# Optimization experiments

Hardware: AMD Instinct MI355X
Metric: run time of the kernel (lower is better)

Reference implementation:

```python
import jax, jax.numpy as jnp
import numpy as np

N_NODES = 10000
N_EDGES = 160000
K = 3  # Chebyshev filter order
DIMS = [(782, 16), (16, 32), (32, 64), (64, 128), (128, 19)]


def _cheb_norm(edge_index, num_nodes):
    # PyG ChebConv norm with normalization='sym', lambda_max=2.0:
    # scaled Laplacian L_hat = 2L/lambda_max - I = -D^{-1/2} A D^{-1/2} (off-diag), diag = 0
    src, dst = edge_index[0], edge_index[1]
    w = jnp.ones(src.shape, dtype=jnp.float32)
    deg = jax.ops.segment_sum(w, src, num_segments=num_nodes)
    dinv = jnp.where(deg > 0, 1.0 / jnp.sqrt(deg), 0.0)  # masked_fill(inf) -> 0
    return -dinv[src] * dinv[dst]


def _spmm(norm, src, dst, x, num_nodes):
    # out[i] = sum_{e: dst[e]==i} norm[e] * x[src[e]]
    return jax.ops.segment_sum(norm[:, None] * x[src], dst, num_segments=num_nodes)


def _cheb_conv(x, src, dst, norm, W, b):
    # W: [K, Fin, Fout]; Chebyshev recursion T0=x, T1=L_hat x, Tk=2 L_hat T_{k-1} - T_{k-2}
    n = x.shape[0]
    Tx0 = x
    out = Tx0 @ W[0]
    Tx1 = _spmm(norm, src, dst, Tx0, n)
    out = out + Tx1 @ W[1]
    for k in range(2, W.shape[0]):
        Tx2 = 2.0 * _spmm(norm, src, dst, Tx1, n) - Tx0
        out = out + Tx2 @ W[k]
        Tx0, Tx1 = Tx1, Tx2
    return out + b


def setup_inputs() -> dict:
    key = jax.random.key(0)
    ks = jax.random.split(key, 2 + len(DIMS))
    x = jax.random.normal(ks[0], (N_NODES, 782), dtype=jnp.float32)
    edge_index = jax.random.randint(ks[1], (2, N_EDGES), 0, N_NODES)
    inp = {"x": x, "edge_index": edge_index}
    for i, (fi, fo) in enumerate(DIMS):
        inp[f"W{i+1}"] = jax.random.normal(ks[2 + i], (K, fi, fo), dtype=jnp.float32) / np.float32(np.sqrt(fi * K))
        inp[f"b{i+1}"] = jnp.zeros((fo,), dtype=jnp.float32)
    return inp


def reference(x, edge_index, W1, b1, W2, b2, W3, b3, W4, b4, W5, b5):
    src, dst = edge_index[0], edge_index[1]
    norm = _cheb_norm(edge_index, x.shape[0])
    h = jax.nn.relu(_cheb_conv(x, src, dst, norm, W1, b1))
    h = jax.nn.relu(_cheb_conv(h, src, dst, norm, W2, b2))
    h = jax.nn.relu(_cheb_conv(h, src, dst, norm, W3, b3))
    h = jax.nn.relu(_cheb_conv(h, src, dst, norm, W4, b4))
    h = _cheb_conv(h, src, dst, norm, W5, b5)
    return jax.nn.softmax(h, axis=-1)
```

## Files before the change

### kernel.cpp

```cpp
#include <hip/hip_runtime.h>
#include <math.h>

#define NN 10000
#define NE 160000
#define CAP 128
#define NT 256
#define WC1_TOTAL (782 * 48)
#define WC5_TOTAL (128 * 60)
#define L1_SPLITS 12
#define L1_KCHUNK 66
#define L1_TN 24
#define L1_RT 4
#define L1_TILES 240
#define CNT_BLKS 625

struct MegaParams {
  const float* x;
  const int* src;
  const int* dst;
  const float* W1; const float* b1;
  const float* W2; const float* b2;
  const float* W3; const float* b3;
  const float* W4; const float* b4;
  const float* W5; const float* b5;
  int* deg; int* cnt; int* bsrc;
  float* dinv; float* wc1; float* wc5;
  float* ABC1; float* E1; float* B2; float* B3; float* B4;
  float* H4; float* ABC5; float* E5; float* P;
  float* out;
};

__device__ __forceinline__ void wcat_one(const float* __restrict__ W,
                                         float* __restrict__ Wc,
                                         int i, int Fin, int F, int Fp) {
  int w3 = 3 * Fp;
  int row = i / w3;
  int c = i - row * w3;
  int sec = c / Fp;
  int f = c - sec * Fp;
  float v = 0.0f;
  if (f < F) {
    if (sec == 0)      v = W[row * F + f] - W[2 * Fin * F + row * F + f];
    else if (sec == 1) v = W[Fin * F + row * F + f];
    else               v = W[2 * Fin * F + row * F + f];
  }
  Wc[i] = v;
}

struct Row8 { float4 lo, hi; };

template <bool AL16>
__device__ __forceinline__ Row8 ld_row8(const float* __restrict__ X, int ldx,
                                        int gr, int M, int kc, int kend) {
  Row8 r;
  r.lo = make_float4(0.f, 0.f, 0.f, 0.f);
  r.hi = make_float4(0.f, 0.f, 0.f, 0.f);
  if (gr < M && kc < kend) {
    const float* xp = X + (size_t)gr * ldx + kc;
    if (kc + 8 <= kend) {
      if (AL16) {
        r.lo = ((const float4*)xp)[0];
        r.hi = ((const float4*)xp)[1];
      } else {
        float2 a = *(const float2*)xp;
        float2 b = *(const float2*)(xp + 2);
        float2 c = *(const float2*)(xp + 4);
        float2 d = *(const float2*)(xp + 6);
        r.lo = make_float4(a.x, a.y, b.x, b.y);
        r.hi = make_float4(c.x, c.y, d.x, d.y);
      }
    } else {
      int rem = kend - kc;
      r.lo.x = xp[0];
      if (rem > 1) r.lo.y = xp[1];
      if (rem > 2) r.lo.z = xp[2];
      if (rem > 3) r.lo.w = xp[3];
      if (rem > 4) r.hi.x = xp[4];
      if (rem > 5) r.hi.y = xp[5];
      if (rem > 6) r.hi.z = xp[6];
    }
  }
  return r;
}

__device__ __forceinline__ float comp8(const Row8& r, int k) {
  switch (k) {
    case 0: return r.lo.x; case 1: return r.lo.y;
    case 2: return r.lo.z; case 3: return r.lo.w;
    case 4: return r.hi.x; case 5: return r.hi.y;
    case 6: return r.hi.z; default: return r.hi.w;
  }
}

template <int TN, int RT, bool AL16, bool DIRECT>
__device__ void gemm_stage(const float* __restrict__ X, int ldx,
                           const float* __restrict__ W, int ldw,
                           float* __restrict__ Y, int ldy,
                           const float* __restrict__ bias, int relu,
                           int M, int Kd, int Nd, int kchunk, int nk,
                           int tile0, int tstride, float* Ws) {
  constexpr int RTILE = NT * RT;
  int ntR = (M + RTILE - 1) / RTILE;
  int ntC = Nd / TN;
  int ntRC = ntR * ntC;
  int ntiles = ntRC * nk;
  constexpr int W4 = TN / 4;
  for (int tile = tile0; tile < ntiles; tile += tstride) {
    int tz = tile / ntRC;
    int rm = tile - tz * ntRC;
    int tc = rm / ntR;
    int tr = rm - tc * ntR;
    int row0 = tr * RTILE;
    int col0 = tc * TN;
    int k0 = tz * kchunk;
    int kend = k0 + kchunk;
    if (kend > Kd) kend = Kd;
    int k8 = ((kend - k0) + 7) & ~7;
    __syncthreads();
    for (int idx = threadIdx.x; idx < k8 * W4; idx += NT) {
      int wk = idx / W4;
      int wc = (idx - wk * W4) * 4;
      float4 wv = make_float4(0.f, 0.f, 0.f, 0.f);
      if (k0 + wk < kend)
        wv = *(const float4*)(W + (size_t)(k0 + wk) * ldw + col0 + wc);
      *(float4*)(Ws + wk * TN + wc) = wv;
    }
    __syncthreads();
    float acc[RT][TN];
#pragma unroll
    for (int i = 0; i < RT; i++)
#pragma unroll
      for (int c = 0; c < TN; c++) acc[i][c] = 0.f;
    int nch = k8 >> 3;
    Row8 cur[RT], nxt[RT];
#pragma unroll
    for (int i = 0; i < RT; i++)
      cur[i] = ld_row8<AL16>(X, ldx, row0 + threadIdx.x + i * NT, M, k0, kend);
    for (int ci = 0; ci < nch; ci++) {
#pragma unroll
      for (int i = 0; i < RT; i++) nxt[i] = cur[i];
      if (ci + 1 < nch) {
#pragma unroll
        for (int i = 0; i < RT; i++)
          nxt[i] = ld_row8<AL16>(X, ldx, row0 + threadIdx.x + i * NT, M,
                                 k0 + (ci + 1) * 8, kend);
      }
      int kb = ci << 3;
#pragma unroll
      for (int k = 0; k < 8; k++) {
        float x0[RT];
#pragma unroll
        for (int i = 0; i < RT; i++) x0[i] = comp8(cur[i], k);
        const float* wr = Ws + (kb + k) * TN;
#pragma unroll
        for (int c = 0; c < TN; c += 4) {
          float4 wv = *(const float4*)(wr + c);
#pragma unroll
          for (int i = 0; i < RT; i++) {
            acc[i][c + 0] += x0[i] * wv.x; acc[i][c + 1] += x0[i] * wv.y;
            acc[i][c + 2] += x0[i] * wv.z; acc[i][c + 3] += x0[i] * wv.w;
          }
        }
      }
#pragma unroll
      for (int i = 0; i < RT; i++) cur[i] = nxt[i];
    }
#pragma unroll
    for (int i = 0; i < RT; i++) {
      int r = row0 + threadIdx.x + i * NT;
      if (r < M) {
        if (DIRECT) {
          float* yr = Y + (size_t)r * ldy + col0;
#pragma unroll
          for (int c = 0; c < TN; c += 4) {
            float4 v;
            v.x = acc[i][c + 0] + (bias ? bias[col0 + c + 0] : 0.f);
            v.y = acc[i][c + 1] + (bias ? bias[col0 + c + 1] : 0.f);
            v.z = acc[i][c + 2] + (bias ? bias[col0 + c + 2] : 0.f);
            v.w = acc[i][c + 3] + (bias ? bias[col0 + c + 3] : 0.f);
            if (relu) {
              v.x = fmaxf(v.x, 0.f); v.y = fmaxf(v.y, 0.f);
              v.z = fmaxf(v.z, 0.f); v.w = fmaxf(v.w, 0.f);
            }
            *(float4*)(yr + c) = v;
          }
        } else {
          float* pr = Y + ((size_t)tz * M + r) * Nd + col0;
#pragma unroll
          for (int c = 0; c < TN; c += 4)
            *(float4*)(pr + c) =
                make_float4(acc[i][c], acc[i][c + 1], acc[i][c + 2], acc[i][c + 3]);
        }
      }
    }
  }
}

__device__ void spmm_stage(const int* __restrict__ cnt,
                           const int* __restrict__ bsrc,
                           const float* __restrict__ dinv,
                           const float* __restrict__ X, int ldx,
                           float* __restrict__ Y, int ldy,
                           const float* __restrict__ add, int lda,
                           const float* __restrict__ bias,
                           float alpha, float beta,
                           int C_log2, int Fstore, int relu, int do_softmax) {
  int wv = threadIdx.x >> 6;
  int lane = threadIdx.x & 63;
  int C = 1 << C_log2;
  int chunk = lane & (C - 1);
  int eslot = lane >> C_log2;
  int Epar = 64 >> C_log2;
  for (int node = blockIdx.x * 4 + wv; node < NN; node += gridDim.x * 4) {
    int cn = cnt[node]; if (cn > CAP) cn = CAP;
    float dn = dinv[node];
    int j0 = node << 7;
    int j1 = j0 + cn;
    float sx = 0.f, sy = 0.f, sz = 0.f, sw = 0.f;
    for (int j = j0 + eslot; j < j1; j += Epar) {
      int sn = bsrc[j];
      float w = dinv[sn];
      float4 xv = *(const float4*)(X + (size_t)sn * ldx + (chunk << 2));
      sx += w * xv.x; sy += w * xv.y; sz += w * xv.z; sw += w * xv.w;
    }
    for (int st = C; st < 64; st <<= 1) {
      sx += __shfl_xor(sx, st);
      sy += __shfl_xor(sy, st);
      sz += __shfl_xor(sz, st);
      sw += __shfl_xor(sw, st);
    }
    if (eslot == 0) {
      float am = -alpha * dn;
      int f0 = chunk << 2;
      float4 u = make_float4(am * sx, am * sy, am * sz, am * sw);
      if (add) {
        float4 av = *(const float4*)(add + (size_t)node * lda + f0);
        u.x += beta * av.x; u.y += beta * av.y; u.z += beta * av.z; u.w += beta * av.w;
      }
      if (bias) {
        if (f0 + 0 < Fstore) u.x += bias[f0 + 0];
        if (f0 + 1 < Fstore) u.y += bias[f0 + 1];
        if (f0 + 2 < Fstore) u.z += bias[f0 + 2];
        if (f0 + 3 < Fstore) u.w += bias[f0 + 3];
      }
      if (!do_softmax) {
        if (relu) {
          u.x = fmaxf(u.x, 0.f); u.y = fmaxf(u.y, 0.f);
          u.z = fmaxf(u.z, 0.f); u.w = fmaxf(u.w, 0.f);
        }
        if (f0 + 4 <= Fstore) {
          *(float4*)(Y + (size_t)node * ldy + f0) = u;
        } else {
          float vv[4] = {u.x, u.y, u.z, u.w};
#pragma unroll
          for (int c = 0; c < 4; c++)
            if (f0 + c < Fstore) Y[(size_t)node * ldy + f0 + c] = vv[c];
        }
      } else {
        float v[4] = {u.x, u.y, u.z, u.w};
        float mx = -INFINITY;
#pragma unroll
        for (int c = 0; c < 4; c++)
          if (f0 + c < Fstore) mx = fmaxf(mx, v[c]);
        mx = fmaxf(mx, __shfl_xor(mx, 1));
        mx = fmaxf(mx, __shfl_xor(mx, 2));
        mx = fmaxf(mx, __shfl_xor(mx, 4));
        float e[4];
        float s = 0.f;
#pragma unroll
        for (int c = 0; c < 4; c++) {
          e[c] = (f0 + c < Fstore) ? __expf(v[c] - mx) : 0.f;
          s += e[c];
        }
        s += __shfl_xor(s, 1);
        s += __shfl_xor(s, 2);
        s += __shfl_xor(s, 4);
        float inv = 1.f / s;
#pragma unroll
        for (int c = 0; c < 4; c++) {
          int f = f0 + c;
          if (f < Fstore) Y[(size_t)node * ldy + f] = e[c] * inv;
        }
      }
    }
  }
}


__global__ __launch_bounds__(NT) void k_zero_wcat(MegaParams p) {
  int tid = blockIdx.x * NT + threadIdx.x;
  int TT = gridDim.x * NT;
  for (int i = tid; i < 2 * NN; i += TT) p.deg[i] = 0;
  for (int i = tid; i < WC1_TOTAL; i += TT) wcat_one(p.W1, p.wc1, i, 782, 16, 16);
  for (int i = tid; i < WC5_TOTAL; i += TT) wcat_one(p.W5, p.wc5, i, 128, 19, 20);
}

__global__ __launch_bounds__(NT) void k_count_gemm1(MegaParams p) {
  __shared__ float Ws[72 * L1_TN];
  if (blockIdx.x < CNT_BLKS) {
    int e = blockIdx.x * NT + threadIdx.x;
    int s = p.src[e], d = p.dst[e];
    atomicAdd(&p.deg[s], 1);
    int slot = atomicAdd(&p.cnt[d], 1);
    if (slot < CAP) p.bsrc[(d << 7) + slot] = s;
  } else {
    gemm_stage<L1_TN, L1_RT, false, false>(p.x, 782, p.wc1, 48, p.P, 0, nullptr, 0,
                                           NN, 782, 48, L1_KCHUNK, L1_SPLITS,
                                           blockIdx.x - CNT_BLKS, 1 << 30, Ws);
  }
}

__global__ __launch_bounds__(NT) void k_reduce_dinv(MegaParams p) {
  int tid = blockIdx.x * NT + threadIdx.x;
  int TT = gridDim.x * NT;
  for (int i = tid; i < NN; i += TT) {
    int d = p.deg[i];
    p.dinv[i] = d > 0 ? 1.0f / sqrtf((float)d) : 0.0f;
  }
  for (int i = tid; i < NN * 48; i += TT) {
    float s = 0.f;
#pragma unroll
    for (int z = 0; z < L1_SPLITS; z++) s += p.P[(size_t)z * (NN * 48) + i];
    p.ABC1[i] = s;
  }
}

__global__ __launch_bounds__(NT) void k_spmm(
    const int* cnt, const int* bsrc, const float* dinv,
    const float* X, int ldx, float* Y, int ldy,
    const float* add, int lda, const float* bias,
    float alpha, float beta, int C_log2, int Fstore, int relu, int do_softmax) {
  spmm_stage(cnt, bsrc, dinv, X, ldx, Y, ldy, add, lda, bias,
             alpha, beta, C_log2, Fstore, relu, do_softmax);
}

__global__ __launch_bounds__(NT, 2) void k_gemm32(
    const float* X, int ldx, const float* W, int ldw, float* Y, int ldy,
    const float* bias, int relu, int Kd, int Nd) {
  __shared__ float Ws[96 * 32];
  gemm_stage<32, 1, true, true>(X, ldx, W, ldw, Y, ldy, bias, relu,
                                NN, Kd, Nd, Kd, 1, blockIdx.x, gridDim.x, Ws);
}
__global__ __launch_bounds__(NT, 2) void k_gemm16(
    const float* X, int ldx, const float* W, int ldw, float* Y, int ldy,
    const float* bias, int relu, int Kd, int Nd) {
  __shared__ float Ws[192 * 16];
  gemm_stage<16, 2, true, true>(X, ldx, W, ldw, Y, ldy, bias, relu,
                                NN, Kd, Nd, Kd, 1, blockIdx.x, gridDim.x, Ws);
}
__global__ __launch_bounds__(NT, 2) void k_gemm20(
    const float* X, int ldx, const float* W, int ldw, float* Y, int ldy,
    const float* bias, int relu, int Kd, int Nd) {
  __shared__ float Ws[128 * 20];
  gemm_stage<20, 1, true, true>(X, ldx, W, ldw, Y, ldy, bias, relu,
                                NN, Kd, Nd, Kd, 1, blockIdx.x, gridDim.x, Ws);
}


extern "C" void kernel_launch(void* const* d_in, const int* in_sizes, int n_in,
                              void* d_out, int out_size, void* d_ws, size_t ws_size,
                              hipStream_t stream) {
  (void)in_sizes; (void)n_in; (void)out_size; (void)ws_size;
  char* p = (char*)d_ws;
  auto alloc = [&](size_t bytes) {
    char* r = p;
    p += (bytes + 255) & ~(size_t)255;
    return r;
  };
  int*   i_deg  = (int*)alloc(sizeof(int) * NN * 2);
  int*   i_bsrc = (int*)alloc(sizeof(int) * NN * CAP);
  float* f_dinv = (float*)alloc(sizeof(float) * NN);
  float* wc1    = (float*)alloc(sizeof(float) * WC1_TOTAL);
  float* wc5    = (float*)alloc(sizeof(float) * WC5_TOTAL);
  float* R1     = (float*)alloc(sizeof(float) * NN * 96);
  float* R2     = (float*)alloc(sizeof(float) * NN * 192);
  float* R3     = (float*)alloc(sizeof(float) * NN * 128);
  float* P      = (float*)alloc(sizeof(float) * NN * 48 * L1_SPLITS);

  MegaParams mp;
  mp.x   = (const float*)d_in[0];
  const int* ei = (const int*)d_in[1];
  mp.src = ei;
  mp.dst = ei + NE;
  mp.W1 = (const float*)d_in[2];  mp.b1 = (const float*)d_in[3];
  mp.W2 = (const float*)d_in[4];  mp.b2 = (const float*)d_in[5];
  mp.W3 = (const float*)d_in[6];  mp.b3 = (const float*)d_in[7];
  mp.W4 = (const float*)d_in[8];  mp.b4 = (const float*)d_in[9];
  mp.W5 = (const float*)d_in[10]; mp.b5 = (const float*)d_in[11];
  mp.deg = i_deg; mp.cnt = i_deg + NN; mp.bsrc = i_bsrc;
  mp.dinv = f_dinv; mp.wc1 = wc1; mp.wc5 = wc5;
  mp.ABC1 = R1; mp.B3 = R1; mp.ABC5 = R1;
  mp.E1 = R2;   mp.B4 = R2; mp.E5 = R2;
  mp.B2 = R3;   mp.H4 = R3;
  mp.P = P;
  mp.out = (float*)d_out;

  k_zero_wcat<<<160, NT, 0, stream>>>(mp);
  k_count_gemm1<<<CNT_BLKS + L1_TILES, NT, 0, stream>>>(mp);
  k_reduce_dinv<<<(NN * 48 + NT - 1) / NT, NT, 0, stream>>>(mp);
  k_spmm<<<2500, NT, 0, stream>>>(mp.cnt, mp.bsrc, mp.dinv, mp.ABC1 + 32, 48,
                                  mp.E1, 16, mp.ABC1 + 16, 48, nullptr,
                                  2.f, 1.f, 2, 16, 0, 0);
  k_spmm<<<2500, NT, 0, stream>>>(mp.cnt, mp.bsrc, mp.dinv, mp.E1, 16,
                                  mp.B2, 48, mp.ABC1, 48, mp.b1,
                                  1.f, 1.f, 2, 16, 1, 0);
  k_spmm<<<2500, NT, 0, stream>>>(mp.cnt, mp.bsrc, mp.dinv, mp.B2, 48,
                                  mp.B2 + 16, 48, nullptr, 0, nullptr,
                                  1.f, 0.f, 2, 16, 0, 0);
  k_spmm<<<2500, NT, 0, stream>>>(mp.cnt, mp.bsrc, mp.dinv, mp.B2 + 16, 48,
                                  mp.B2 + 32, 48, mp.B2, 48, nullptr,
                                  2.f, -1.f, 2, 16, 0, 0);
  k_gemm32<<<40, NT, 0, stream>>>(mp.B2, 48, mp.W2, 32, mp.B3, 96, mp.b2, 1, 48, 32);
  k_spmm<<<2500, NT, 0, stream>>>(mp.cnt, mp.bsrc, mp.dinv, mp.B3, 96,
                                  mp.B3 + 32, 96, nullptr, 0, nullptr,
                                  1.f, 0.f, 3, 32, 0, 0);
  k_spmm<<<2500, NT, 0, stream>>>(mp.cnt, mp.bsrc, mp.dinv, mp.B3 + 32, 96,
                                  mp.B3 + 64, 96, mp.B3, 96, nullptr,
                                  2.f, -1.f, 3, 32, 0, 0);
  k_gemm32<<<80, NT, 0, stream>>>(mp.B3, 96, mp.W3, 64, mp.B4, 192, mp.b3, 1, 96, 64);
  k_spmm<<<2500, NT, 0, stream>>>(mp.cnt, mp.bsrc, mp.dinv, mp.B4, 192,
                                  mp.B4 + 64, 192, nullptr, 0, nullptr,
                                  1.f, 0.f, 4, 64, 0, 0);
  k_spmm<<<2500, NT, 0, stream>>>(mp.cnt, mp.bsrc, mp.dinv, mp.B4 + 64, 192,
                                  mp.B4 + 128, 192, mp.B4, 192, nullptr,
                                  2.f, -1.f, 4, 64, 0, 0);
  k_gemm16<<<160, NT, 0, stream>>>(mp.B4, 192, mp.W4, 128, mp.H4, 128, mp.b4, 1,
                                   192, 128);
  k_gemm20<<<120, NT, 0, stream>>>(mp.H4, 128, mp.wc5, 60, mp.ABC5, 60, nullptr, 0,
                                   128, 60);
  k_spmm<<<2500, NT, 0, stream>>>(mp.cnt, mp.bsrc, mp.dinv, mp.ABC5 + 40, 60,
                                  mp.E5, 32, mp.ABC5 + 20, 60, nullptr,
                                  2.f, 1.f, 3, 20, 0, 0);
  k_spmm<<<2500, NT, 0, stream>>>(mp.cnt, mp.bsrc, mp.dinv, mp.E5, 32,
                                  mp.out, 19, mp.ABC5, 60, mp.b5,
                                  1.f, 1.f, 3, 19, 0, 1);
}
```

Before: 288.7 us.

## Replace layer-1 GEMM with register-resident readlane kernel and retile gemm16

The first-layer x·Wcat GEMM (782→48) now uses a dedicated routine. Each wave owns 12 output columns and 4 rows per lane, broadcasts weights across lanes with readlane instead of staging them in shared memory, and double-buffers the X and W loads in registers. The K split goes from 12 chunks of 66 to 13 chunks of 64, which gives more tiles. Separately, gemm16 drops to one row per thread and launches twice as many blocks. The readlane broadcasts add scalar-path instructions, and the register pressure of the 48 accumulators may limit occupancy.

```diff
diff --git a/kernel.cpp b/kernel.cpp
--- a/kernel.cpp
+++ b/kernel.cpp
@@ -7,11 +7,9 @@
 #define NT 256
 #define WC1_TOTAL (782 * 48)
 #define WC5_TOTAL (128 * 60)
-#define L1_SPLITS 12
-#define L1_KCHUNK 66
-#define L1_TN 24
-#define L1_RT 4
-#define L1_TILES 240
+#define L1_SPLITS 13
+#define L1_KCHUNK 64
+#define L1_TILES (40 * L1_SPLITS)
 #define CNT_BLKS 625
 
 struct MegaParams {
@@ -89,6 +87,93 @@
     case 2: return r.lo.z; case 3: return r.lo.w;
     case 4: return r.hi.x; case 5: return r.hi.y;
     case 6: return r.hi.z; default: return r.hi.w;
+  }
+}
+
+__device__ __forceinline__ float rlane(float v, int i) {
+  return __int_as_float(__builtin_amdgcn_readlane(__float_as_int(v), i));
+}
+
+__device__ __forceinline__ float2 ldw8(const float* __restrict__ Wf, int kb,
+                                       int col0, int lc, int lk) {
+  float2 w = make_float2(0.f, 0.f);
+  if (lc < 12) {
+    int k1 = kb + lk, k2 = kb + 4 + lk;
+    if (k1 < 782) w.x = Wf[k1 * 48 + col0 + lc];
+    if (k2 < 782) w.y = Wf[k2 * 48 + col0 + lc];
+  }
+  return w;
+}
+
+__device__ void gemm1_rl(const float* __restrict__ X,
+                         const float* __restrict__ Wf,
+                         float* __restrict__ P,
+                         int tile0, int tstride) {
+  const int ntR = 40;
+  int wid  = threadIdx.x >> 6;
+  int lane = threadIdx.x & 63;
+  int col0 = wid * 12;
+  int lc = lane & 15;
+  int lk = lane >> 4;
+  for (int tile = tile0; tile < ntR * L1_SPLITS; tile += tstride) {
+    int tz = tile / ntR;
+    int tr = tile - tz * ntR;
+    int row0 = tr * 256;
+    int k0 = tz * L1_KCHUNK;
+    int kend = k0 + L1_KCHUNK;
+    if (kend > 782) kend = 782;
+    int nch = ((kend - k0) + 7) >> 3;
+    float acc[4][12];
+#pragma unroll
+    for (int i = 0; i < 4; i++)
+#pragma unroll
+      for (int c = 0; c < 12; c++) acc[i][c] = 0.f;
+    Row8 cur[4], nxt[4];
+    float2 wcur, wnxt;
+#pragma unroll
+    for (int i = 0; i < 4; i++)
+      cur[i] = ld_row8<false>(X, 782, row0 + lane + 64 * i, NN, k0, kend);
+    wcur = ldw8(Wf, k0, col0, lc, lk);
+    for (int ci = 0; ci < nch; ci++) {
+      if (ci + 1 < nch) {
+        int kc2 = k0 + (ci + 1) * 8;
+#pragma unroll
+        for (int i = 0; i < 4; i++)
+          nxt[i] = ld_row8<false>(X, 782, row0 + lane + 64 * i, NN, kc2, kend);
+        wnxt = ldw8(Wf, kc2, col0, lc, lk);
+      }
+#pragma unroll
+      for (int kin = 0; kin < 8; kin++) {
+        float x0 = comp8(cur[0], kin);
+        float x1 = comp8(cur[1], kin);
+        float x2 = comp8(cur[2], kin);
+        float x3 = comp8(cur[3], kin);
+        float wsrc = (kin < 4) ? wcur.x : wcur.y;
+#pragma unroll
+        for (int c = 0; c < 12; c++) {
+          float w = rlane(wsrc, (kin & 3) * 16 + c);
+          acc[0][c] += x0 * w;
+          acc[1][c] += x1 * w;
+          acc[2][c] += x2 * w;
+          acc[3][c] += x3 * w;
+        }
+      }
+      if (ci + 1 < nch) {
+#pragma unroll
+        for (int i = 0; i < 4; i++) cur[i] = nxt[i];
+        wcur = wnxt;
+      }
+    }
+#pragma unroll
+    for (int i = 0; i < 4; i++) {
+      int r = row0 + lane + 64 * i;
+      if (r < NN) {
+        float* pr = P + ((size_t)tz * NN + r) * 48 + col0;
+        *(float4*)(pr + 0) = make_float4(acc[i][0], acc[i][1], acc[i][2], acc[i][3]);
+        *(float4*)(pr + 4) = make_float4(acc[i][4], acc[i][5], acc[i][6], acc[i][7]);
+        *(float4*)(pr + 8) = make_float4(acc[i][8], acc[i][9], acc[i][10], acc[i][11]);
+      }
+    }
   }
 }
 
@@ -296,7 +381,6 @@
 }
 
 __global__ __launch_bounds__(NT) void k_count_gemm1(MegaParams p) {
-  __shared__ float Ws[72 * L1_TN];
   if (blockIdx.x < CNT_BLKS) {
     int e = blockIdx.x * NT + threadIdx.x;
     int s = p.src[e], d = p.dst[e];
@@ -304,9 +388,7 @@
     int slot = atomicAdd(&p.cnt[d], 1);
     if (slot < CAP) p.bsrc[(d << 7) + slot] = s;
   } else {
-    gemm_stage<L1_TN, L1_RT, false, false>(p.x, 782, p.wc1, 48, p.P, 0, nullptr, 0,
-                                           NN, 782, 48, L1_KCHUNK, L1_SPLITS,
-                                           blockIdx.x - CNT_BLKS, 1 << 30, Ws);
+    gemm1_rl(p.x, p.wc1, p.P, blockIdx.x - CNT_BLKS, 1 << 30);
   }
 }
 
@@ -345,7 +427,7 @@
     const float* X, int ldx, const float* W, int ldw, float* Y, int ldy,
     const float* bias, int relu, int Kd, int Nd) {
   __shared__ float Ws[192 * 16];
-  gemm_stage<16, 2, true, true>(X, ldx, W, ldw, Y, ldy, bias, relu,
+  gemm_stage<16, 1, true, true>(X, ldx, W, ldw, Y, ldy, bias, relu,
                                 NN, Kd, Nd, Kd, 1, blockIdx.x, gridDim.x, Ws);
 }
 __global__ __launch_bounds__(NT, 2) void k_gemm20(
@@ -424,7 +506,7 @@
   k_spmm<<<2500, NT, 0, stream>>>(mp.cnt, mp.bsrc, mp.dinv, mp.B4 + 64, 192,
                                   mp.B4 + 128, 192, mp.B4, 192, nullptr,
                                   2.f, -1.f, 4, 64, 0, 0);
-  k_gemm16<<<160, NT, 0, stream>>>(mp.B4, 192, mp.W4, 128, mp.H4, 128, mp.b4, 1,
+  k_gemm16<<<320, NT, 0, stream>>>(mp.B4, 192, mp.W4, 128, mp.H4, 128, mp.b4, 1,
                                    192, 128);
   k_gemm20<<<120, NT, 0, stream>>>(mp.H4, 128, mp.wc5, 60, mp.ABC5, 60, nullptr, 0,
                                    128, 60);
```

New measurement: 275.2 us. 1.05x faster.

## Fuse final Chebyshev SpMM with dense GEMM for layers 2 and 3

Applied to the files above, without the earlier changes.

Adds a fused kernel that computes the T2 SpMM for a node in one wavefront and immediately multiplies the full [T0,T1,T2] row by the weight matrix using readlane broadcasts, applying bias and ReLU. This replaces a separate SpMM and GEMM launch per layer, removing a launch and an intermediate round trip through global memory. It also retunes the layer-1 split-K GEMM to full-width 48-column tiles with twice the blocks, and halves the row tile of the layer-4 GEMM while doubling its grid. The fused kernel keeps each weight column in registers and runs a serial per-node FMA chain, so occupancy and per-node latency may suffer.

```diff
diff --git a/kernel.cpp b/kernel.cpp
--- a/kernel.cpp
+++ b/kernel.cpp
@@ -9,9 +9,6 @@
 #define WC5_TOTAL (128 * 60)
 #define L1_SPLITS 12
 #define L1_KCHUNK 66
-#define L1_TN 24
-#define L1_RT 4
-#define L1_TILES 240
 #define CNT_BLKS 625
 
 struct MegaParams {
@@ -90,6 +87,10 @@
     case 4: return r.hi.x; case 5: return r.hi.y;
     case 6: return r.hi.z; default: return r.hi.w;
   }
+}
+
+__device__ __forceinline__ float rlane(float v, int i) {
+  return __int_as_float(__builtin_amdgcn_readlane(__float_as_int(v), i));
 }
 
 template <int TN, int RT, bool AL16, bool DIRECT>
@@ -286,6 +287,66 @@
   }
 }
 
+template <int F, int C_log2, int LD, int KK, int FOUT, int LDO>
+__global__ __launch_bounds__(NT) void k_fused_t2gemm(
+    const int* __restrict__ cnt, const int* __restrict__ bsrc,
+    const float* __restrict__ dinv, const float* __restrict__ B,
+    const float* __restrict__ W, const float* __restrict__ bias,
+    float* __restrict__ Y) {
+  int wv = threadIdx.x >> 6;
+  int lane = threadIdx.x & 63;
+  constexpr int C = 1 << C_log2;
+  int chunk = lane & (C - 1);
+  int eslot = lane >> C_log2;
+  constexpr int Epar = 64 >> C_log2;
+  int col = lane % FOUT;
+  float wr[KK];
+#pragma unroll
+  for (int k = 0; k < KK; k++) wr[k] = W[k * FOUT + col];
+  float bb = bias[col];
+  for (int node = blockIdx.x * 4 + wv; node < NN; node += gridDim.x * 4) {
+    int cn = cnt[node]; if (cn > CAP) cn = CAP;
+    float dn = dinv[node];
+    int j0 = node << 7, j1 = j0 + cn;
+    float sx = 0.f, sy = 0.f, sz = 0.f, sw = 0.f;
+    for (int j = j0 + eslot; j < j1; j += Epar) {
+      int sn = bsrc[j];
+      float w = dinv[sn];
+      float4 xv = *(const float4*)(B + (size_t)sn * LD + F + (chunk << 2));
+      sx += w * xv.x; sy += w * xv.y; sz += w * xv.z; sw += w * xv.w;
+    }
+#pragma unroll
+    for (int st = C; st < 64; st <<= 1) {
+      sx += __shfl_xor(sx, st);
+      sy += __shfl_xor(sy, st);
+      sz += __shfl_xor(sz, st);
+      sw += __shfl_xor(sw, st);
+    }
+    int ridx = (lane < 2 * F) ? lane : (lane - 2 * F);
+    float rv0 = B[(size_t)node * LD + ridx];
+    int f = (KK == 48) ? (lane - 2 * F) : lane;
+    int cc = (f >> 2) & (C - 1);
+    float a0 = __shfl(sx, cc), a1 = __shfl(sy, cc);
+    float a2 = __shfl(sz, cc), a3 = __shfl(sw, cc);
+    int comp = f & 3;
+    float Ssel = (comp == 0) ? a0 : (comp == 1) ? a1 : (comp == 2) ? a2 : a3;
+    float t2v = fmaf(-2.f * dn, Ssel, -rv0);
+    float acc = bb;
+    if (KK == 48) {
+      float rv = (lane < 2 * F) ? rv0 : t2v;
+#pragma unroll
+      for (int k = 0; k < 48; k++) acc = fmaf(rlane(rv, k), wr[k], acc);
+    } else {
+#pragma unroll
+      for (int k = 0; k < 64; k++) acc = fmaf(rlane(rv0, k), wr[k], acc);
+#pragma unroll
+      for (int k = 64; k < 96; k++) acc = fmaf(rlane(t2v, k - 64), wr[k], acc);
+    }
+    acc = fmaxf(acc, 0.f);
+    if (lane < FOUT) Y[(size_t)node * LDO + col] = acc;
+  }
+}
+
 
 __global__ __launch_bounds__(NT) void k_zero_wcat(MegaParams p) {
   int tid = blockIdx.x * NT + threadIdx.x;
@@ -296,7 +357,7 @@
 }
 
 __global__ __launch_bounds__(NT) void k_count_gemm1(MegaParams p) {
-  __shared__ float Ws[72 * L1_TN];
+  __shared__ float Ws[72 * 48];
   if (blockIdx.x < CNT_BLKS) {
     int e = blockIdx.x * NT + threadIdx.x;
     int s = p.src[e], d = p.dst[e];
@@ -304,9 +365,9 @@
     int slot = atomicAdd(&p.cnt[d], 1);
     if (slot < CAP) p.bsrc[(d << 7) + slot] = s;
   } else {
-    gemm_stage<L1_TN, L1_RT, false, false>(p.x, 782, p.wc1, 48, p.P, 0, nullptr, 0,
-                                           NN, 782, 48, L1_KCHUNK, L1_SPLITS,
-                                           blockIdx.x - CNT_BLKS, 1 << 30, Ws);
+    gemm_stage<48, 1, false, false>(p.x, 782, p.wc1, 48, p.P, 0, nullptr, 0,
+                                    NN, 782, 48, L1_KCHUNK, L1_SPLITS,
+                                    blockIdx.x - CNT_BLKS, 1 << 30, Ws);
   }
 }
 
@@ -334,18 +395,11 @@
              alpha, beta, C_log2, Fstore, relu, do_softmax);
 }
 
-__global__ __launch_bounds__(NT, 2) void k_gemm32(
-    const float* X, int ldx, const float* W, int ldw, float* Y, int ldy,
-    const float* bias, int relu, int Kd, int Nd) {
-  __shared__ float Ws[96 * 32];
-  gemm_stage<32, 1, true, true>(X, ldx, W, ldw, Y, ldy, bias, relu,
-                                NN, Kd, Nd, Kd, 1, blockIdx.x, gridDim.x, Ws);
-}
 __global__ __launch_bounds__(NT, 2) void k_gemm16(
     const float* X, int ldx, const float* W, int ldw, float* Y, int ldy,
     const float* bias, int relu, int Kd, int Nd) {
   __shared__ float Ws[192 * 16];
-  gemm_stage<16, 2, true, true>(X, ldx, W, ldw, Y, ldy, bias, relu,
+  gemm_stage<16, 1, true, true>(X, ldx, W, ldw, Y, ldy, bias, relu,
                                 NN, Kd, Nd, Kd, 1, blockIdx.x, gridDim.x, Ws);
 }
 __global__ __launch_bounds__(NT, 2) void k_gemm20(
@@ -396,7 +450,7 @@
   mp.out = (float*)d_out;
 
   k_zero_wcat<<<160, NT, 0, stream>>>(mp);
-  k_count_gemm1<<<CNT_BLKS + L1_TILES, NT, 0, stream>>>(mp);
+  k_count_gemm1<<<CNT_BLKS + 480, NT, 0, stream>>>(mp);
   k_reduce_dinv<<<(NN * 48 + NT - 1) / NT, NT, 0, stream>>>(mp);
   k_spmm<<<2500, NT, 0, stream>>>(mp.cnt, mp.bsrc, mp.dinv, mp.ABC1 + 32, 48,
                                   mp.E1, 16, mp.ABC1 + 16, 48, nullptr,
@@ -407,24 +461,20 @@
   k_spmm<<<2500, NT, 0, stream>>>(mp.cnt, mp.bsrc, mp.dinv, mp.B2, 48,
                                   mp.B2 + 16, 48, nullptr, 0, nullptr,
                                   1.f, 0.f, 2, 16, 0, 0);
-  k_spmm<<<2500, NT, 0, stream>>>(mp.cnt, mp.bsrc, mp.dinv, mp.B2 + 16, 48,
-                                  mp.B2 + 32, 48, mp.B2, 48, nullptr,
-                                  2.f, -1.f, 2, 16, 0, 0);
-  k_gemm32<<<40, NT, 0, stream>>>(mp.B2, 48, mp.W2, 32, mp.B3, 96, mp.b2, 1, 48, 32);
+  k_fused_t2gemm<16, 2, 48, 48, 32, 96><<<1250, NT, 0, stream>>>(
+      mp.cnt, mp.bsrc, mp.dinv, mp.B2, mp.W2, mp.b2, mp.B3);
   k_spmm<<<2500, NT, 0, stream>>>(mp.cnt, mp.bsrc, mp.dinv, mp.B3, 96,
                                   mp.B3 + 32, 96, nullptr, 0, nullptr,
                                   1.f, 0.f, 3, 32, 0, 0);
-  k_spmm<<<2500, NT, 0, stream>>>(mp.cnt, mp.bsrc, mp.dinv, mp.B3 + 32, 96,
-                                  mp.B3 + 64, 96, mp.B3, 96, nullptr,
-                                  2.f, -1.f, 3, 32, 0, 0);
-  k_gemm32<<<80, NT, 0, stream>>>(mp.B3, 96, mp.W3, 64, mp.B4, 192, mp.b3, 1, 96, 64);
+  k_fused_t2gemm<32, 3, 96, 96, 64, 192><<<1250, NT, 0, stream>>>(
+      mp.cnt, mp.bsrc, mp.dinv, mp.B3, mp.W3, mp.b3, mp.B4);
   k_spmm<<<2500, NT, 0, stream>>>(mp.cnt, mp.bsrc, mp.dinv, mp.B4, 192,
                                   mp.B4 + 64, 192, nullptr, 0, nullptr,
                                   1.f, 0.f, 4, 64, 0, 0);
   k_spmm<<<2500, NT, 0, stream>>>(mp.cnt, mp.bsrc, mp.dinv, mp.B4 + 64, 192,
                                   mp.B4 + 128, 192, mp.B4, 192, nullptr,
                                   2.f, -1.f, 4, 64, 0, 0);
-  k_gemm16<<<160, NT, 0, stream>>>(mp.B4, 192, mp.W4, 128, mp.H4, 128, mp.b4, 1,
+  k_gemm16<<<320, NT, 0, stream>>>(mp.B4, 192, mp.W4, 128, mp.H4, 128, mp.b4, 1,
                                    192, 128);
   k_gemm20<<<120, NT, 0, stream>>>(mp.H4, 128, mp.wc5, 60, mp.ABC5, 60, nullptr, 0,
                                    128, 60);
```

Result: faster. 265.6 us (-8.0%).
